# Kernel optimization log

Hardware: AMD Instinct MI355X
Metric: run time of the kernel (lower is better)

Reference implementation:

```python
import jax, jax.numpy as jnp
import numpy as np

N_NODES = 50000


def _norm_adj(num_nodes, edge_index):
    # Append self loops, compute symmetric normalization values per edge.
    row, col = edge_index[0], edge_index[1]
    loop = jnp.arange(num_nodes, dtype=edge_index.dtype)
    row = jnp.concatenate([row, loop])
    col = jnp.concatenate([col, loop])
    ones = jnp.ones(row.shape[0], dtype=jnp.float32)
    deg = jax.ops.segment_sum(ones, row, num_segments=num_nodes)  # row-sum of A (duplicates summed, as coalesce does)
    dinv = jnp.clip(deg, 1.0) ** -0.5
    v = dinv[row] * dinv[col]  # [E + N]
    return row, col, v


def _spmm(row, col, v, x, num_nodes):
    # y[i] = sum_{e: row[e]=i} v[e] * x[col[e]]  (duplicate edges sum, matching coalesced sparse mm)
    return jax.ops.segment_sum(v[:, None] * x[col], row, num_segments=num_nodes)


def setup_inputs() -> dict:
    key = jax.random.key(0)
    ks = jax.random.split(key, 6)
    in_dim, hidden_dim, out_dim = 128, 256, 128
    n_edges = 800000
    x = jax.random.normal(ks[0], (N_NODES, in_dim), dtype=jnp.float32)
    edge_index = jax.random.randint(ks[1], (2, n_edges), 0, N_NODES, dtype=jnp.int32)
    W1 = jax.random.normal(ks[2], (hidden_dim, in_dim), dtype=jnp.float32) * (1.0 / np.sqrt(in_dim))
    b1 = jax.random.normal(ks[3], (hidden_dim,), dtype=jnp.float32) * 0.01
    W2 = jax.random.normal(ks[4], (out_dim, hidden_dim), dtype=jnp.float32) * (1.0 / np.sqrt(hidden_dim))
    b2 = jax.random.normal(ks[5], (out_dim,), dtype=jnp.float32) * 0.01
    return {"x": x, "edge_index": edge_index, "W1": W1, "b1": b1, "W2": W2, "b2": b2}


def reference(x, edge_index, W1, b1, W2, b2):
    n = x.shape[0]
    row, col, v = _norm_adj(n, edge_index)
    h = _spmm(row, col, v, x, n)            # A @ x
    h = jax.nn.relu(h @ W1.T + b1)           # lin1 + relu (dropout is eval no-op)
    h = _spmm(row, col, v, h, n)             # A @ h
    return h @ W2.T + b2                     # lin2
```

## Files before the change

kernel.cpp:

```cpp
#include <hip/hip_runtime.h>
#include <hip/hip_bf16.h>

#define NNODES 50000
#define DIM 128
#define NBUCK 196

typedef unsigned short u16;
typedef _Float16 f16;
typedef float  f32x4  __attribute__((ext_vector_type(4)));
typedef _Float16 f16x4v __attribute__((ext_vector_type(4)));
typedef _Float16 f16x8 __attribute__((ext_vector_type(8)));

#define MFMAH(a, b, c) __builtin_amdgcn_mfma_f32_16x16x32_f16((a), (b), (c), 0, 0, 0)

__global__ void f32_to_f16(const float* __restrict__ in, f16* __restrict__ out, int n4) {
    int i = blockIdx.x * blockDim.x + threadIdx.x;
    if (i < n4) {
        float4 v = reinterpret_cast<const float4*>(in)[i];
        f16x4v o = { (f16)v.x, (f16)v.y, (f16)v.z, (f16)v.w };
        reinterpret_cast<f16x4v*>(out)[i] = o;
    }
}

__global__ __launch_bounds__(256) void bucket_hist(const int* __restrict__ row,
                                                   int* __restrict__ bcnt, int nE) {
    __shared__ int hist[256];
    int t = threadIdx.x;
    hist[t] = 0;
    __syncthreads();
    int base_e = blockIdx.x * 2048 + t;
    #pragma unroll
    for (int k = 0; k < 8; ++k) {
        int e = base_e + k * 256;
        if (e < nE) atomicAdd(&hist[(unsigned)row[e] >> 8], 1);
    }
    __syncthreads();
    if (hist[t] > 0) atomicAdd(&bcnt[t], hist[t]);
}

__global__ __launch_bounds__(256) void bucket_scan(const int* __restrict__ bcnt,
                                                   int* __restrict__ bbase,
                                                   int* __restrict__ gcursor, int nb) {
    __shared__ int sc[256];
    int t = threadIdx.x;
    int v = (t < nb) ? bcnt[t] : 0;
    sc[t] = v;
    __syncthreads();
    for (int off = 1; off < 256; off <<= 1) {
        int u = (t >= off) ? sc[t - off] : 0;
        __syncthreads();
        sc[t] += u;
        __syncthreads();
    }
    if (t < nb) {
        int excl = sc[t] - v;
        bbase[t] = excl;
        gcursor[t] = excl;
    }
    if (t == 255) bbase[nb] = sc[255];
}

__global__ __launch_bounds__(256) void bucket_place(const int* __restrict__ row,
                                                    const int* __restrict__ col,
                                                    int* __restrict__ gcursor,
                                                    unsigned* __restrict__ bkt, int nE) {
    __shared__ int hist[256];
    __shared__ int cur[256];
    int t = threadIdx.x;
    hist[t] = 0;
    __syncthreads();
    unsigned pk[8]; int valid = 0;
    int base_e = blockIdx.x * 2048 + t;
    #pragma unroll
    for (int k = 0; k < 8; ++k) {
        int e = base_e + k * 256;
        if (e < nE) {
            unsigned r = (unsigned)row[e], c = (unsigned)col[e];
            pk[k] = (r << 16) | c;
            valid |= 1 << k;
            atomicAdd(&hist[r >> 8], 1);
        }
    }
    __syncthreads();
    if (hist[t] > 0) cur[t] = atomicAdd(&gcursor[t], hist[t]);
    __syncthreads();
    #pragma unroll
    for (int k = 0; k < 8; ++k) {
        if (valid & (1 << k)) {
            int pos = atomicAdd(&cur[pk[k] >> 24], 1);
            bkt[pos] = pk[k];
        }
    }
}

__global__ __launch_bounds__(256) void csr_fill(const unsigned* __restrict__ bkt,
                                                const int* __restrict__ bbase,
                                                int* __restrict__ row_ptr,
                                                float* __restrict__ dinv,
                                                u16* __restrict__ cols16, int n) {
    __shared__ int lcnt[256], lscan[256], lcur[256];
    int b = blockIdx.x, t = threadIdx.x;
    int r0 = b << 8;
    int s = bbase[b], e = bbase[b + 1];
    lcnt[t] = 0;
    __syncthreads();
    for (int i = s + t; i < e; i += 256)
        atomicAdd(&lcnt[(bkt[i] >> 16) & 255], 1);
    __syncthreads();
    int v = lcnt[t];
    lscan[t] = v;
    __syncthreads();
    for (int off = 1; off < 256; off <<= 1) {
        int u = (t >= off) ? lscan[t - off] : 0;
        __syncthreads();
        lscan[t] += u;
        __syncthreads();
    }
    int gpos = s + lscan[t] - v;
    int r = r0 + t;
    if (r < n) {
        row_ptr[r] = gpos;
        dinv[r] = rsqrtf((float)(v + 1));
    }
    if (r == n) row_ptr[n] = gpos;
    lcur[t] = gpos;
    __syncthreads();
    for (int i = s + t; i < e; i += 256) {
        unsigned rc = bkt[i];
        int pos = atomicAdd(&lcur[(rc >> 16) & 255], 1);
        cols16[pos] = (u16)(rc & 0xffffu);
    }
}

template <bool OUT16, bool BIAS>
__global__ __launch_bounds__(256) void spmm_csr_h(const int* __restrict__ row_ptr,
                         const u16* __restrict__ cols16,
                         const f16* __restrict__ Xh, const float* __restrict__ dinv,
                         const float* __restrict__ bias,
                         float* __restrict__ Y, f16* __restrict__ Yh, int n) {
    int tid = blockIdx.x * blockDim.x + threadIdx.x;
    int i = tid >> 5;
    int l = tid & 31;
    if (i >= n) return;
    const f16x4v* X4 = reinterpret_cast<const f16x4v*>(Xh);
    float di = dinv[i];
    f16x4v xv = X4[(size_t)i * 32 + l];
    float4 acc;
    acc.x = di * (float)xv[0]; acc.y = di * (float)xv[1];
    acc.z = di * (float)xv[2]; acc.w = di * (float)xv[3];
    int s = row_ptr[i], e = row_ptr[i + 1];
    for (int j = s; j < e; j += 8) {
        int c[8]; bool ok[8];
        #pragma unroll
        for (int t = 0; t < 8; ++t) {
            int idx = j + t;
            ok[t] = idx < e;
            c[t] = (int)cols16[ok[t] ? idx : (e - 1)];
        }
        f16x4v g[8];
        #pragma unroll
        for (int t = 0; t < 8; ++t) g[t] = X4[(size_t)c[t] * 32 + l];
        float w[8];
        #pragma unroll
        for (int t = 0; t < 8; ++t) w[t] = ok[t] ? dinv[c[t]] : 0.f;
        #pragma unroll
        for (int t = 0; t < 8; ++t) {
            acc.x += w[t] * (float)g[t][0];
            acc.y += w[t] * (float)g[t][1];
            acc.z += w[t] * (float)g[t][2];
            acc.w += w[t] * (float)g[t][3];
        }
    }
    acc.x *= di; acc.y *= di; acc.z *= di; acc.w *= di;
    if (BIAS) {
        float4 b = reinterpret_cast<const float4*>(bias)[l];
        acc.x += b.x; acc.y += b.y; acc.z += b.z; acc.w += b.w;
    }
    if (OUT16) {
        f16x4v o = { (f16)acc.x, (f16)acc.y, (f16)acc.z, (f16)acc.w };
        *reinterpret_cast<f16x4v*>(&Yh[(size_t)i * DIM + l * 4]) = o;
    } else {
        reinterpret_cast<float4*>(Y)[(size_t)i * 32 + l] = acc;
    }
}

__global__ __launch_bounds__(256, 2) void mlp_fused(
        const f16* __restrict__ y1, const f16* __restrict__ w1,
        const float* __restrict__ b1, const f16* __restrict__ w2,
        f16* __restrict__ z, int M) {
    constexpr int HSTR = 264;
    __shared__ f16 hl[4][32][HSTR];
    const int wave = threadIdx.x >> 6;
    const int lane = threadIdx.x & 63;
    const int lr = lane & 15;
    const int lq = lane >> 4;
    const int mbase = blockIdx.x * 128 + wave * 32;

    f16x8 yb[2][4];
    #pragma unroll
    for (int nf = 0; nf < 2; ++nf) {
        int r = min(mbase + nf * 16 + lr, M - 1);
        const f16* pr = y1 + (size_t)r * 128 + lq * 8;
        #pragma unroll
        for (int ks = 0; ks < 4; ++ks)
            yb[nf][ks] = *reinterpret_cast<const f16x8*>(pr + ks * 32);
    }

    #pragma unroll 1
    for (int q = 0; q < 4; ++q) {
        const int hc0 = q * 64;
        f16x8 wa[4][4];
        #pragma unroll
        for (int mf = 0; mf < 4; ++mf) {
            const f16* pw = w1 + (size_t)(hc0 + mf * 16 + lr) * 128 + lq * 8;
            #pragma unroll
            for (int ks = 0; ks < 4; ++ks)
                wa[mf][ks] = *reinterpret_cast<const f16x8*>(pw + ks * 32);
        }
        f32x4 acc[4][2] = {};
        #pragma unroll
        for (int ks = 0; ks < 4; ++ks)
            #pragma unroll
            for (int mf = 0; mf < 4; ++mf)
                #pragma unroll
                for (int nf = 0; nf < 2; ++nf)
                    acc[mf][nf] = MFMAH(wa[mf][ks], yb[nf][ks], acc[mf][nf]);
        #pragma unroll
        for (int mf = 0; mf < 4; ++mf) {
            float4 bb = *reinterpret_cast<const float4*>(&b1[hc0 + mf * 16 + lq * 4]);
            #pragma unroll
            for (int nf = 0; nf < 2; ++nf) {
                f16x4v hv = { (f16)fmaxf(acc[mf][nf][0] + bb.x, 0.f),
                              (f16)fmaxf(acc[mf][nf][1] + bb.y, 0.f),
                              (f16)fmaxf(acc[mf][nf][2] + bb.z, 0.f),
                              (f16)fmaxf(acc[mf][nf][3] + bb.w, 0.f) };
                *reinterpret_cast<f16x4v*>(&hl[wave][nf * 16 + lr][hc0 + mf * 16 + lq * 4]) = hv;
            }
        }
    }

    f32x4 acc2[8][2] = {};
    #pragma unroll 1
    for (int ks = 0; ks < 8; ++ks) {
        f16x8 hb[2];
        #pragma unroll
        for (int nf = 0; nf < 2; ++nf)
            hb[nf] = *reinterpret_cast<const f16x8*>(&hl[wave][nf * 16 + lr][ks * 32 + lq * 8]);
        f16x8 wa2[8];
        #pragma unroll
        for (int mf = 0; mf < 8; ++mf)
            wa2[mf] = *reinterpret_cast<const f16x8*>(w2 + (size_t)(mf * 16 + lr) * 256 + ks * 32 + lq * 8);
        #pragma unroll
        for (int mf = 0; mf < 8; ++mf)
            #pragma unroll
            for (int nf = 0; nf < 2; ++nf)
                acc2[mf][nf] = MFMAH(wa2[mf], hb[nf], acc2[mf][nf]);
    }
    #pragma unroll
    for (int nf = 0; nf < 2; ++nf) {
        int node = mbase + nf * 16 + lr;
        if (node >= M) continue;
        #pragma unroll
        for (int mf = 0; mf < 8; ++mf) {
            f16x4v zv = { (f16)acc2[mf][nf][0], (f16)acc2[mf][nf][1],
                          (f16)acc2[mf][nf][2], (f16)acc2[mf][nf][3] };
            *reinterpret_cast<f16x4v*>(z + (size_t)node * 128 + mf * 16 + lq * 4) = zv;
        }
    }
}

extern "C" void kernel_launch(void* const* d_in, const int* in_sizes, int n_in,
                              void* d_out, int out_size, void* d_ws, size_t ws_size,
                              hipStream_t stream) {
    const float* x  = (const float*)d_in[0];
    const int*   ei = (const int*)d_in[1];
    const float* W1 = (const float*)d_in[2];
    const float* b1 = (const float*)d_in[3];
    const float* W2 = (const float*)d_in[4];
    const float* b2 = (const float*)d_in[5];
    float* out = (float*)d_out;

    const int N = NNODES;
    const int E = in_sizes[1] / 2;
    const int IN_D = 128, HID = 256;
    const int* row = ei;
    const int* col = ei + E;

    char* ws = (char*)d_ws;
    size_t off = 0;
    auto carve = [&](size_t bytes) { void* p = ws + off; off += (bytes + 255) & ~size_t(255); return p; };
    int*      bcnt    = (int*)carve((size_t)256 * 4);
    int*      bbase   = (int*)carve((size_t)(NBUCK + 1) * 4);
    int*      gcursor = (int*)carve((size_t)256 * 4);
    int*      row_ptr = (int*)carve((size_t)(N + 1) * 4);
    float*    dinv    = (float*)carve((size_t)N * 4);
    unsigned* bkt     = (unsigned*)carve((size_t)E * 4);
    u16*      cols16  = (u16*)carve((size_t)E * 2);
    f16*      w1h     = (f16*)carve((size_t)HID * IN_D * 2);
    f16*      w2h     = (f16*)carve((size_t)IN_D * HID * 2);
    f16*      xh      = (f16*)carve((size_t)N * IN_D * 2);
    f16*      y1h     = (f16*)carve((size_t)N * IN_D * 2);
    f16*      zh      = y1h;

    const int TB = 256;
    const int eblk = (E + 2047) / 2048;

    hipMemsetAsync(bcnt, 0, 256 * 4, stream);
    bucket_hist<<<eblk, TB, 0, stream>>>(row, bcnt, E);
    bucket_scan<<<1, TB, 0, stream>>>(bcnt, bbase, gcursor, NBUCK);
    bucket_place<<<eblk, TB, 0, stream>>>(row, col, gcursor, bkt, E);
    csr_fill<<<NBUCK, TB, 0, stream>>>(bkt, bbase, row_ptr, dinv, cols16, N);

    f32_to_f16<<<((HID * IN_D / 4) + TB - 1) / TB, TB, 0, stream>>>(W1, w1h, HID * IN_D / 4);
    f32_to_f16<<<((IN_D * HID / 4) + TB - 1) / TB, TB, 0, stream>>>(W2, w2h, IN_D * HID / 4);
    f32_to_f16<<<((N * IN_D / 4) + TB - 1) / TB, TB, 0, stream>>>(x, xh, N * IN_D / 4);

    spmm_csr_h<true, false><<<(N * 32 + TB - 1) / TB, TB, 0, stream>>>(
        row_ptr, cols16, xh, dinv, nullptr, nullptr, y1h, N);

    mlp_fused<<<(N + 127) / 128, 256, 0, stream>>>(y1h, w1h, b1, w2h, zh, N);

    spmm_csr_h<false, true><<<(N * 32 + TB - 1) / TB, TB, 0, stream>>>(
        row_ptr, cols16, zh, dinv, b2, out, nullptr, N);
}
```

Before: 159.2 us.

## Pre-scale gather sources by dinv and pad with zero row to drop per-edge weights

Folds the source-side dinv scaling into the fp16 feature tables: x is scaled during conversion and the MLP output is scaled before being stored. The SpMM then only sums gathered rows and no longer loads dinv[col] per edge. Out-of-range edges point to an extra zero padding row instead of being masked, and the gather loop is unrolled to 16. The three conversion kernels are merged into one launch and the memset is replaced by a tiny kernel. In exchange, the dinv factor is rounded to fp16 together with the features.

```diff
diff --git a/kernel.cpp b/kernel.cpp
--- a/kernel.cpp
+++ b/kernel.cpp
@@ -13,13 +13,8 @@
 
 #define MFMAH(a, b, c) __builtin_amdgcn_mfma_f32_16x16x32_f16((a), (b), (c), 0, 0, 0)
 
-__global__ void f32_to_f16(const float* __restrict__ in, f16* __restrict__ out, int n4) {
-    int i = blockIdx.x * blockDim.x + threadIdx.x;
-    if (i < n4) {
-        float4 v = reinterpret_cast<const float4*>(in)[i];
-        f16x4v o = { (f16)v.x, (f16)v.y, (f16)v.z, (f16)v.w };
-        reinterpret_cast<f16x4v*>(out)[i] = o;
-    }
+__global__ void zero256(int* __restrict__ p) {
+    p[threadIdx.x] = 0;
 }
 
 __global__ __launch_bounds__(256) void bucket_hist(const int* __restrict__ row,
@@ -132,43 +127,75 @@
     }
 }
 
+__global__ __launch_bounds__(256) void prep_tables(
+        const float* __restrict__ W1, const float* __restrict__ W2,
+        const float* __restrict__ x, const float* __restrict__ dinv,
+        f16* __restrict__ w1h, f16* __restrict__ w2h,
+        f16* __restrict__ xs, f16* __restrict__ zs, int n) {
+    const int WQ = (256 * 128) / 4;
+    const int XQ = n * (DIM / 4);
+    int i = blockIdx.x * 256 + threadIdx.x;
+    if (i < WQ) {
+        float4 v = reinterpret_cast<const float4*>(W1)[i];
+        f16x4v o = { (f16)v.x, (f16)v.y, (f16)v.z, (f16)v.w };
+        reinterpret_cast<f16x4v*>(w1h)[i] = o;
+    } else if (i < 2 * WQ) {
+        int j = i - WQ;
+        float4 v = reinterpret_cast<const float4*>(W2)[j];
+        f16x4v o = { (f16)v.x, (f16)v.y, (f16)v.z, (f16)v.w };
+        reinterpret_cast<f16x4v*>(w2h)[j] = o;
+    } else {
+        int j = i - 2 * WQ;
+        if (j < XQ) {
+            float d = dinv[j >> 5];
+            float4 v = reinterpret_cast<const float4*>(x)[j];
+            f16x4v o = { (f16)(d * v.x), (f16)(d * v.y), (f16)(d * v.z), (f16)(d * v.w) };
+            reinterpret_cast<f16x4v*>(xs)[j] = o;
+        } else if (j < XQ + 32) {
+            f16x4v o = {};
+            reinterpret_cast<f16x4v*>(xs)[j] = o;
+        } else if (j < XQ + 64) {
+            f16x4v o = {};
+            reinterpret_cast<f16x4v*>(zs)[XQ + (j - XQ - 32)] = o;
+        }
+    }
+}
+
 template <bool OUT16, bool BIAS>
-__global__ __launch_bounds__(256) void spmm_csr_h(const int* __restrict__ row_ptr,
+__global__ __launch_bounds__(256) void spmm_gather(const int* __restrict__ row_ptr,
                          const u16* __restrict__ cols16,
-                         const f16* __restrict__ Xh, const float* __restrict__ dinv,
+                         const f16* __restrict__ Xs, const float* __restrict__ dinv,
                          const float* __restrict__ bias,
                          float* __restrict__ Y, f16* __restrict__ Yh, int n) {
     int tid = blockIdx.x * blockDim.x + threadIdx.x;
     int i = tid >> 5;
     int l = tid & 31;
     if (i >= n) return;
-    const f16x4v* X4 = reinterpret_cast<const f16x4v*>(Xh);
+    const f16x4v* X4 = reinterpret_cast<const f16x4v*>(Xs);
     float di = dinv[i];
     f16x4v xv = X4[(size_t)i * 32 + l];
     float4 acc;
-    acc.x = di * (float)xv[0]; acc.y = di * (float)xv[1];
-    acc.z = di * (float)xv[2]; acc.w = di * (float)xv[3];
+    acc.x = (float)xv[0]; acc.y = (float)xv[1];
+    acc.z = (float)xv[2]; acc.w = (float)xv[3];
     int s = row_ptr[i], e = row_ptr[i + 1];
-    for (int j = s; j < e; j += 8) {
-        int c[8]; bool ok[8];
-        #pragma unroll
-        for (int t = 0; t < 8; ++t) {
+    for (int j = s; j < e; j += 16) {
+        int c[16];
+        #pragma unroll
+        for (int t = 0; t < 16; ++t) {
             int idx = j + t;
-            ok[t] = idx < e;
-            c[t] = (int)cols16[ok[t] ? idx : (e - 1)];
-        }
-        f16x4v g[8];
-        #pragma unroll
-        for (int t = 0; t < 8; ++t) g[t] = X4[(size_t)c[t] * 32 + l];
-        float w[8];
-        #pragma unroll
-        for (int t = 0; t < 8; ++t) w[t] = ok[t] ? dinv[c[t]] : 0.f;
-        #pragma unroll
-        for (int t = 0; t < 8; ++t) {
-            acc.x += w[t] * (float)g[t][0];
-            acc.y += w[t] * (float)g[t][1];
-            acc.z += w[t] * (float)g[t][2];
-            acc.w += w[t] * (float)g[t][3];
+            bool ok = idx < e;
+            int cc = (int)cols16[ok ? idx : (e - 1)];
+            c[t] = ok ? cc : n;
+        }
+        f16x4v g[16];
+        #pragma unroll
+        for (int t = 0; t < 16; ++t) g[t] = X4[(size_t)c[t] * 32 + l];
+        #pragma unroll
+        for (int t = 0; t < 16; ++t) {
+            acc.x += (float)g[t][0];
+            acc.y += (float)g[t][1];
+            acc.z += (float)g[t][2];
+            acc.w += (float)g[t][3];
         }
     }
     acc.x *= di; acc.y *= di; acc.z *= di; acc.w *= di;
@@ -187,7 +214,7 @@
 __global__ __launch_bounds__(256, 2) void mlp_fused(
         const f16* __restrict__ y1, const f16* __restrict__ w1,
         const float* __restrict__ b1, const f16* __restrict__ w2,
-        f16* __restrict__ z, int M) {
+        const float* __restrict__ dinv, f16* __restrict__ zs, int M) {
     constexpr int HSTR = 264;
     __shared__ f16 hl[4][32][HSTR];
     const int wave = threadIdx.x >> 6;
@@ -260,11 +287,12 @@
     for (int nf = 0; nf < 2; ++nf) {
         int node = mbase + nf * 16 + lr;
         if (node >= M) continue;
+        float dn = dinv[node];
         #pragma unroll
         for (int mf = 0; mf < 8; ++mf) {
-            f16x4v zv = { (f16)acc2[mf][nf][0], (f16)acc2[mf][nf][1],
-                          (f16)acc2[mf][nf][2], (f16)acc2[mf][nf][3] };
-            *reinterpret_cast<f16x4v*>(z + (size_t)node * 128 + mf * 16 + lq * 4) = zv;
+            f16x4v zv = { (f16)(dn * acc2[mf][nf][0]), (f16)(dn * acc2[mf][nf][1]),
+                          (f16)(dn * acc2[mf][nf][2]), (f16)(dn * acc2[mf][nf][3]) };
+            *reinterpret_cast<f16x4v*>(zs + (size_t)node * 128 + mf * 16 + lq * 4) = zv;
         }
     }
 }
@@ -298,28 +326,30 @@
     u16*      cols16  = (u16*)carve((size_t)E * 2);
     f16*      w1h     = (f16*)carve((size_t)HID * IN_D * 2);
     f16*      w2h     = (f16*)carve((size_t)IN_D * HID * 2);
-    f16*      xh      = (f16*)carve((size_t)N * IN_D * 2);
-    f16*      y1h     = (f16*)carve((size_t)N * IN_D * 2);
-    f16*      zh      = y1h;
+    f16*      xs      = (f16*)carve((size_t)(N + 1) * IN_D * 2);
+    f16*      y1h     = (f16*)carve((size_t)(N + 1) * IN_D * 2);
+    f16*      zsh     = y1h;
 
     const int TB = 256;
     const int eblk = (E + 2047) / 2048;
 
-    hipMemsetAsync(bcnt, 0, 256 * 4, stream);
+    zero256<<<1, 256, 0, stream>>>(bcnt);
     bucket_hist<<<eblk, TB, 0, stream>>>(row, bcnt, E);
     bucket_scan<<<1, TB, 0, stream>>>(bcnt, bbase, gcursor, NBUCK);
     bucket_place<<<eblk, TB, 0, stream>>>(row, col, gcursor, bkt, E);
     csr_fill<<<NBUCK, TB, 0, stream>>>(bkt, bbase, row_ptr, dinv, cols16, N);
 
-    f32_to_f16<<<((HID * IN_D / 4) + TB - 1) / TB, TB, 0, stream>>>(W1, w1h, HID * IN_D / 4);
-    f32_to_f16<<<((IN_D * HID / 4) + TB - 1) / TB, TB, 0, stream>>>(W2, w2h, IN_D * HID / 4);
-    f32_to_f16<<<((N * IN_D / 4) + TB - 1) / TB, TB, 0, stream>>>(x, xh, N * IN_D / 4);
-
-    spmm_csr_h<true, false><<<(N * 32 + TB - 1) / TB, TB, 0, stream>>>(
-        row_ptr, cols16, xh, dinv, nullptr, nullptr, y1h, N);
-
-    mlp_fused<<<(N + 127) / 128, 256, 0, stream>>>(y1h, w1h, b1, w2h, zh, N);
-
-    spmm_csr_h<false, true><<<(N * 32 + TB - 1) / TB, TB, 0, stream>>>(
-        row_ptr, cols16, zh, dinv, b2, out, nullptr, N);
-}
+    {
+        int total_q = 2 * (HID * IN_D / 4) + N * (DIM / 4) + 64;
+        prep_tables<<<(total_q + TB - 1) / TB, TB, 0, stream>>>(
+            W1, W2, x, dinv, w1h, w2h, xs, zsh, N);
+    }
+
+    spmm_gather<true, false><<<(N * 32 + TB - 1) / TB, TB, 0, stream>>>(
+        row_ptr, cols16, xs, dinv, nullptr, nullptr, y1h, N);
+
+    mlp_fused<<<(N + 127) / 128, 256, 0, stream>>>(y1h, w1h, b1, w2h, dinv, zsh, N);
+
+    spmm_gather<false, true><<<(N * 32 + TB - 1) / TB, TB, 0, stream>>>(
+        row_ptr, cols16, zsh, dinv, b2, out, nullptr, N);
+}
```

New measurement: 155.4 us. -2.4%, faster.
